# Optimization experiments

Measured on AMD Instinct MI355X. Metric: run time of the kernel, lower is better.

The kernel has to match this reference:

```python
import jax, jax.numpy as jnp
import numpy as np


def setup_inputs() -> dict:
    key = jax.random.key(0)
    B, N, D = 32, 1024, 1024
    x = jax.random.normal(key, (B, N, D), dtype=jnp.float32)
    return {"x": x}


def reference(x) -> jnp.ndarray:
    # query = key = value = x (the module's Linear layers are unused).
    # kl_divs[b,i,j] = KL(softmax(x[b,i]) || softmax(x[b,j])) for i != j, 0 on diag.
    # Since KL(p||p) == 0, the full vectorized KL matrix matches the looped version.
    logp = jax.nn.log_softmax(x, axis=-1)          # [B, N, D]
    p = jnp.exp(logp)                               # softmax(x)
    neg_ent = jnp.sum(p * logp, axis=-1)            # [B, N]  = sum p log p
    cross = jnp.einsum('bid,bjd->bij', p, logp)     # [B, N, N] = sum_d p_i log q_j
    kl = neg_ent[:, :, None] - cross                # [B, N, N]
    attn = jax.nn.softmax(-kl, axis=-1)             # [B, N, N]
    out = jnp.einsum('bij,bjd->bid', attn, x)       # value = x
    return out
```

## Files before the change

kernel.cpp:

```cpp
#include <hip/hip_runtime.h>
#include <hip/hip_bf16.h>
#include <stdint.h>

#define B_ 32
#define N_ 1024
#define D_ 1024

typedef __bf16 bf16x8 __attribute__((ext_vector_type(8)));
typedef float f32x4 __attribute__((ext_vector_type(4)));

static __device__ __forceinline__ unsigned short f2bf(float f) {
    union { float f; unsigned u; } v; v.f = f;
    unsigned r = v.u + 0x7fffu + ((v.u >> 16) & 1u);
    return (unsigned short)(r >> 16);
}

static __device__ __forceinline__ void gld_lds16(const void* g, void* l) {
    __builtin_amdgcn_global_load_lds(
        (const __attribute__((address_space(1))) void*)g,
        (__attribute__((address_space(3))) void*)l, 16, 0, 0);
}

__global__ __launch_bounds__(256) void prep_kernel(const float* __restrict__ x,
        unsigned short* __restrict__ pb, unsigned short* __restrict__ xb,
        float* __restrict__ lse) {
    int row  = blockIdx.x * 4 + (threadIdx.x >> 6);
    int lane = threadIdx.x & 63;
    const float4* xr = (const float4*)(x + (size_t)row * D_);

    float4 v[4];
    #pragma unroll
    for (int q = 0; q < 4; q++) v[q] = xr[lane + 64 * q];

    float m = -1e30f;
    #pragma unroll
    for (int q = 0; q < 4; q++)
        m = fmaxf(m, fmaxf(fmaxf(v[q].x, v[q].y), fmaxf(v[q].z, v[q].w)));
    #pragma unroll
    for (int o = 1; o < 64; o <<= 1) m = fmaxf(m, __shfl_xor(m, o, 64));

    float4 e[4];
    float s = 0.0f;
    #pragma unroll
    for (int q = 0; q < 4; q++) {
        e[q].x = __expf(v[q].x - m); e[q].y = __expf(v[q].y - m);
        e[q].z = __expf(v[q].z - m); e[q].w = __expf(v[q].w - m);
        s += e[q].x + e[q].y + e[q].z + e[q].w;
    }
    #pragma unroll
    for (int o = 1; o < 64; o <<= 1) s += __shfl_xor(s, o, 64);
    float inv = 1.0f / s;

    ushort4* pr = (ushort4*)(pb + (size_t)row * D_);
    ushort4* xw = (ushort4*)(xb + (size_t)row * D_);
    #pragma unroll
    for (int q = 0; q < 4; q++) {
        ushort4 pu, xu;
        pu.x = f2bf(e[q].x * inv); pu.y = f2bf(e[q].y * inv);
        pu.z = f2bf(e[q].z * inv); pu.w = f2bf(e[q].w * inv);
        xu.x = f2bf(v[q].x); xu.y = f2bf(v[q].y);
        xu.z = f2bf(v[q].z); xu.w = f2bf(v[q].w);
        pr[lane + 64 * q] = pu;
        xw[lane + 64 * q] = xu;
    }
    if (lane == 0) lse[row] = m + logf(s);
}

#define SB0() __builtin_amdgcn_sched_barrier(0)

#define STEP(tt, bvC, a0C, bvN, a0N)                                            \
  {                                                                             \
    int brN = (brC == 2) ? 0 : brC + 1;                                         \
    int bw  = (brN == 2) ? 0 : brN + 1;                                         \
    asm volatile("s_waitcnt lgkmcnt(4)" ::: "memory");                          \
    SB0();                                                                      \
    __builtin_amdgcn_s_setprio(1);                                              \
    _Pragma("unroll") for (int i2 = 0; i2 < 4; ++i2)                            \
    _Pragma("unroll") for (int j = 0; j < 4; ++j)                               \
      acc[i2][j] = __builtin_amdgcn_mfma_f32_16x16x32_bf16(a0C[i2], bvC[j],     \
                                                           acc[i2][j], 0, 0, 0);\
    __builtin_amdgcn_s_setprio(0);                                              \
    if ((tt) + 2 < 32) stage(bw, (tt) + 2);                                     \
    asm volatile("s_waitcnt lgkmcnt(0)" ::: "memory");                          \
    if ((tt) < 30)        asm volatile("s_waitcnt vmcnt(4)" ::: "memory");      \
    else if ((tt) == 30)  asm volatile("s_waitcnt vmcnt(0)" ::: "memory");      \
    SB0();                                                                      \
    __builtin_amdgcn_s_barrier();                                               \
    SB0();                                                                      \
    if ((tt) + 1 < 32) {                                                        \
      _Pragma("unroll") for (int j = 0; j < 4; ++j)  bvN[j]  = lB(brN, j);      \
      _Pragma("unroll") for (int i2 = 0; i2 < 4; ++i2) a0N[i2] = lA(brN, 0, i2);\
    }                                                                           \
    SB0();                                                                      \
    __builtin_amdgcn_s_setprio(1);                                              \
    _Pragma("unroll") for (int i2 = 0; i2 < 4; ++i2)                            \
    _Pragma("unroll") for (int j = 0; j < 4; ++j)                               \
      acc[4 + i2][j] = __builtin_amdgcn_mfma_f32_16x16x32_bf16(a1[i2], bvC[j],  \
                                                        acc[4 + i2][j], 0, 0, 0);\
    __builtin_amdgcn_s_setprio(0);                                              \
    if ((tt) + 1 < 32) {                                                        \
      _Pragma("unroll") for (int i2 = 0; i2 < 4; ++i2) a1[i2] = lA(brN, 1, i2); \
    }                                                                           \
    brC = brN;                                                                  \
  }

template<int MODE>
__global__ __launch_bounds__(512, 2) void gemm_bt(const unsigned short* __restrict__ Ag,
        const unsigned short* __restrict__ Bg, void* __restrict__ Cg,
        const float* __restrict__ lse, float* __restrict__ rowsum) {
    const int K = 1024;
    int b = blockIdx.z;
    const unsigned short* A  = Ag + (size_t)b * N_ * K;
    const unsigned short* Bm = Bg + (size_t)b * N_ * K;
    int m0 = blockIdx.y * 256, n0 = blockIdx.x * 256;

    extern __shared__ char lds[];

    int t = threadIdx.x;
    int wave = t >> 6, lane = t & 63;
    int wr = wave >> 2, wc = wave & 3;
    int fm = lane & 15, gf = lane >> 4;

    f32x4 acc[8][4];
    #pragma unroll
    for (int i = 0; i < 8; i++)
        #pragma unroll
        for (int j = 0; j < 4; j++)
            #pragma unroll
            for (int r = 0; r < 4; r++) acc[i][j][r] = 0.0f;

    int rr = t >> 2, s = t & 3;
    int sg = s ^ ((rr >> 1) & 3);
    int rbase = rr + (rr & 64);
    int row0s = rbase;
    int row1s = 64 + rbase;
    const unsigned short* pA0 = A  + (size_t)(m0 + row0s) * K + sg * 8;
    const unsigned short* pA1 = A  + (size_t)(m0 + row1s) * K + sg * 8;
    const unsigned short* pB0 = Bm + (size_t)(n0 + row0s) * K + sg * 8;
    const unsigned short* pB1 = Bm + (size_t)(n0 + row1s) * K + sg * 8;
    int dA0 = row0s * 64 + s * 16;
    int dA1 = row1s * 64 + s * 16;

    auto stage = [&](int bw, int tg) {
        char* ab = lds + bw * 16384;
        char* bb = lds + 49152 + bw * 16384;
        gld_lds16(pA0 + tg * 32, ab + dA0);
        gld_lds16(pA1 + tg * 32, ab + dA1);
        gld_lds16(pB0 + tg * 32, bb + dA0);
        gld_lds16(pB1 + tg * 32, bb + dA1);
    };

    int slot = (gf ^ ((fm >> 1) & 3)) * 16;
    int arow = wr * 128 + fm;
    int brow = wc * 64 + fm;

    auto lA = [&](int br, int q, int i2) {
        return *(const bf16x8*)(lds + br * 16384 + (arow + q * 64 + i2 * 16) * 64 + slot);
    };
    auto lB = [&](int br, int j) {
        return *(const bf16x8*)(lds + 49152 + br * 16384 + (brow + j * 16) * 64 + slot);
    };

    bf16x8 bvA[4], a0A[4], bvB[4], a0B[4], a1[4];

    stage(0, 0);
    stage(1, 1);
    asm volatile("s_waitcnt vmcnt(4)" ::: "memory");
    __builtin_amdgcn_s_barrier();
    SB0();
    #pragma unroll
    for (int j = 0; j < 4; ++j)  bvA[j]  = lB(0, j);
    #pragma unroll
    for (int i2 = 0; i2 < 4; ++i2) a0A[i2] = lA(0, 0, i2);
    SB0();
    #pragma unroll
    for (int i2 = 0; i2 < 4; ++i2) a1[i2] = lA(0, 1, i2);

    int brC = 0;
    for (int tp = 0; tp < 16; ++tp) {
        STEP(2 * tp,     bvA, a0A, bvB, a0B);
        STEP(2 * tp + 1, bvB, a0B, bvA, a0A);
    }

    int cr = (lane >> 4) * 4;
    int cc = lane & 15;

    if (MODE == 0) {
        unsigned short* Co = (unsigned short*)Cg + (size_t)b * (size_t)N_ * N_;
        float lsev[4];
        #pragma unroll
        for (int j = 0; j < 4; j++) lsev[j] = lse[b * N_ + n0 + wc * 64 + j * 16 + cc];
        float rsum[32];
        #pragma unroll
        for (int q = 0; q < 32; q++) rsum[q] = 0.0f;
        #pragma unroll
        for (int i = 0; i < 8; i++) {
            #pragma unroll
            for (int r = 0; r < 4; r++) {
                int row = m0 + wr * 128 + i * 16 + cr + r;
                size_t ro = (size_t)row * N_;
                #pragma unroll
                for (int j = 0; j < 4; j++) {
                    int col = n0 + wc * 64 + j * 16 + cc;
                    float ev = __expf(acc[i][j][r] - lsev[j]);
                    unsigned short eb = f2bf(ev);
                    union { unsigned u; float f; } bk; bk.u = ((unsigned)eb) << 16;
                    Co[ro + col] = eb;
                    rsum[i * 4 + r] += bk.f;
                }
            }
        }
        #pragma unroll
        for (int q = 0; q < 32; q++) {
            float sv = rsum[q];
            sv += __shfl_xor(sv, 1, 64);
            sv += __shfl_xor(sv, 2, 64);
            sv += __shfl_xor(sv, 4, 64);
            sv += __shfl_xor(sv, 8, 64);
            rsum[q] = sv;
        }
        if (cc == 0) {
            #pragma unroll
            for (int q = 0; q < 32; q++) {
                int row = m0 + wr * 128 + (q >> 2) * 16 + cr + (q & 3);
                atomicAdd(&rowsum[b * N_ + row], rsum[q]);
            }
        }
    } else {
        float* Co = (float*)Cg + (size_t)b * (size_t)N_ * N_;
        #pragma unroll
        for (int i = 0; i < 8; i++) {
            #pragma unroll
            for (int r = 0; r < 4; r++) {
                int row = m0 + wr * 128 + i * 16 + cr + r;
                float inv = 1.0f / rowsum[b * N_ + row];
                size_t ro = (size_t)row * N_;
                #pragma unroll
                for (int j = 0; j < 4; j++) {
                    int col = n0 + wc * 64 + j * 16 + cc;
                    Co[ro + col] = acc[i][j][r] * inv;
                }
            }
        }
    }
}

__global__ __launch_bounds__(256) void transpose_kernel(const unsigned short* __restrict__ in,
        unsigned short* __restrict__ out) {
    int b  = blockIdx.z;
    int j0 = blockIdx.y * 64;
    int d0 = blockIdx.x * 64;
    __shared__ unsigned short tile[64][66];
    const unsigned short* ip = in + ((size_t)b * N_ + j0) * D_ + d0;
    int t = threadIdx.x;
    #pragma unroll
    for (int c = t; c < 512; c += 256) {
        int r = c >> 3, col = (c & 7) * 8;
        uint4 val = *(const uint4*)(ip + (size_t)r * D_ + col);
        unsigned int* dst = (unsigned int*)&tile[r][col];
        dst[0] = val.x; dst[1] = val.y; dst[2] = val.z; dst[3] = val.w;
    }
    __syncthreads();
    unsigned short* op = out + ((size_t)b * D_ + d0) * N_ + j0;
    #pragma unroll
    for (int c = t; c < 512; c += 256) {
        int r = c >> 3, col = (c & 7) * 8;
        unsigned short vals[8];
        #pragma unroll
        for (int k = 0; k < 8; k++) vals[k] = tile[col + k][r];
        uint4 o;
        o.x = (unsigned)vals[0] | ((unsigned)vals[1] << 16);
        o.y = (unsigned)vals[2] | ((unsigned)vals[3] << 16);
        o.z = (unsigned)vals[4] | ((unsigned)vals[5] << 16);
        o.w = (unsigned)vals[6] | ((unsigned)vals[7] << 16);
        *(uint4*)(op + (size_t)r * N_ + col) = o;
    }
}

extern "C" void kernel_launch(void* const* d_in, const int* in_sizes, int n_in,
                              void* d_out, int out_size, void* d_ws, size_t ws_size,
                              hipStream_t stream) {
    const float* x = (const float*)d_in[0];
    float* out = (float*)d_out;
    char* ws = (char*)d_ws;

    unsigned short* pb    = (unsigned short*)(ws);
    unsigned short* xb    = (unsigned short*)(ws + 67108864ULL);
    unsigned short* xbT   = (unsigned short*)(ws + 134217728ULL);
    unsigned short* attnE = (unsigned short*)(ws + 201326592ULL);
    float*          lse   = (float*)(ws + 268435456ULL);
    float*          rowsum= (float*)(ws + 268566528ULL);

    hipMemsetAsync(rowsum, 0, B_ * N_ * sizeof(float), stream);
    prep_kernel<<<dim3(B_ * N_ / 4), 256, 0, stream>>>(x, pb, xb, lse);
    transpose_kernel<<<dim3(16, 16, B_), 256, 0, stream>>>(xb, xbT);
    gemm_bt<0><<<dim3(4, 4, B_), 512, 98304, stream>>>(pb, xb, attnE, lse, rowsum);
    gemm_bt<1><<<dim3(4, 4, B_), 512, 98304, stream>>>(attnE, xbT, out, nullptr, rowsum);
}
```

Measured before the change: 420.3 us.

## Restructure GEMM mainloop to 4-stage LDS pipeline with split A/B staging and XCD-aware block remap

The GEMM mainloop moves from a 3-buffer ring with register double-buffering to a 4-buffer LDS ring with three tiles prefetched, and splits each tile's A and B global-to-LDS loads across the two MFMA halves. It adds extra barriers per tile and drops register double buffering, so it relies on deeper prefetch to hide latency. Block indices are also remapped so that blocks sharing a batch land on the same XCD (h&7 interleave), which should improve L2 reuse. LDS usage grows to 128KB per block, which at 2 blocks per CU may limit occupancy.

```diff
diff --git a/kernel.cpp b/kernel.cpp
--- a/kernel.cpp
+++ b/kernel.cpp
@@ -67,41 +67,43 @@
 }
 
 #define SB0() __builtin_amdgcn_sched_barrier(0)
-
-#define STEP(tt, bvC, a0C, bvN, a0N)                                            \
+#define VM8 asm volatile("s_waitcnt vmcnt(8)" ::: "memory")
+#define VM4 asm volatile("s_waitcnt vmcnt(4)" ::: "memory")
+#define VM0 asm volatile("s_waitcnt vmcnt(0)" ::: "memory")
+#define VMN
+
+#define TILE(tt, rB, wB, DOSTAGE, VM)                                           \
   {                                                                             \
-    int brN = (brC == 2) ? 0 : brC + 1;                                         \
-    int bw  = (brN == 2) ? 0 : brN + 1;                                         \
-    asm volatile("s_waitcnt lgkmcnt(4)" ::: "memory");                          \
+    _Pragma("unroll") for (int j = 0; j < 4; ++j)  bv[j] = lB(rB, j);           \
+    _Pragma("unroll") for (int i2 = 0; i2 < 4; ++i2) a0[i2] = lA(rB, 0, i2);    \
+    if (DOSTAGE) stageA(wB, (tt) + 3);                                          \
+    SB0();                                                                      \
+    __builtin_amdgcn_s_barrier();                                               \
+    asm volatile("s_waitcnt lgkmcnt(0)" ::: "memory");                          \
     SB0();                                                                      \
     __builtin_amdgcn_s_setprio(1);                                              \
     _Pragma("unroll") for (int i2 = 0; i2 < 4; ++i2)                            \
-    _Pragma("unroll") for (int j = 0; j < 4; ++j)                               \
-      acc[i2][j] = __builtin_amdgcn_mfma_f32_16x16x32_bf16(a0C[i2], bvC[j],     \
-                                                           acc[i2][j], 0, 0, 0);\
+      _Pragma("unroll") for (int j = 0; j < 4; ++j)                             \
+        acc[i2][j] = __builtin_amdgcn_mfma_f32_16x16x32_bf16(a0[i2], bv[j],     \
+                                                             acc[i2][j], 0, 0, 0); \
     __builtin_amdgcn_s_setprio(0);                                              \
-    if ((tt) + 2 < 32) stage(bw, (tt) + 2);                                     \
+    SB0();                                                                      \
+    __builtin_amdgcn_s_barrier();                                               \
+    _Pragma("unroll") for (int i2 = 0; i2 < 4; ++i2) a1[i2] = lA(rB, 1, i2);    \
+    if (DOSTAGE) stageB(wB, (tt) + 3);                                          \
+    VM;                                                                         \
+    SB0();                                                                      \
+    __builtin_amdgcn_s_barrier();                                               \
     asm volatile("s_waitcnt lgkmcnt(0)" ::: "memory");                          \
-    if ((tt) < 30)        asm volatile("s_waitcnt vmcnt(4)" ::: "memory");      \
-    else if ((tt) == 30)  asm volatile("s_waitcnt vmcnt(0)" ::: "memory");      \
-    SB0();                                                                      \
-    __builtin_amdgcn_s_barrier();                                               \
-    SB0();                                                                      \
-    if ((tt) + 1 < 32) {                                                        \
-      _Pragma("unroll") for (int j = 0; j < 4; ++j)  bvN[j]  = lB(brN, j);      \
-      _Pragma("unroll") for (int i2 = 0; i2 < 4; ++i2) a0N[i2] = lA(brN, 0, i2);\
-    }                                                                           \
     SB0();                                                                      \
     __builtin_amdgcn_s_setprio(1);                                              \
     _Pragma("unroll") for (int i2 = 0; i2 < 4; ++i2)                            \
-    _Pragma("unroll") for (int j = 0; j < 4; ++j)                               \
-      acc[4 + i2][j] = __builtin_amdgcn_mfma_f32_16x16x32_bf16(a1[i2], bvC[j],  \
-                                                        acc[4 + i2][j], 0, 0, 0);\
+      _Pragma("unroll") for (int j = 0; j < 4; ++j)                             \
+        acc[4 + i2][j] = __builtin_amdgcn_mfma_f32_16x16x32_bf16(a1[i2], bv[j], \
+                                                        acc[4 + i2][j], 0, 0, 0); \
     __builtin_amdgcn_s_setprio(0);                                              \
-    if ((tt) + 1 < 32) {                                                        \
-      _Pragma("unroll") for (int i2 = 0; i2 < 4; ++i2) a1[i2] = lA(brN, 1, i2); \
-    }                                                                           \
-    brC = brN;                                                                  \
+    SB0();                                                                      \
+    __builtin_amdgcn_s_barrier();                                               \
   }
 
 template<int MODE>
@@ -109,10 +111,15 @@
         const unsigned short* __restrict__ Bg, void* __restrict__ Cg,
         const float* __restrict__ lse, float* __restrict__ rowsum) {
     const int K = 1024;
-    int b = blockIdx.z;
+
+    int h = blockIdx.x + 4 * blockIdx.y + 16 * blockIdx.z;
+    int l = (h & 7) * 64 + (h >> 3);
+    int b  = l >> 4;
+    int m0 = ((l >> 2) & 3) * 256;
+    int n0 = (l & 3) * 256;
+
     const unsigned short* A  = Ag + (size_t)b * N_ * K;
     const unsigned short* Bm = Bg + (size_t)b * N_ * K;
-    int m0 = blockIdx.y * 256, n0 = blockIdx.x * 256;
 
     extern __shared__ char lds[];
 
@@ -131,56 +138,53 @@
 
     int rr = t >> 2, s = t & 3;
     int sg = s ^ ((rr >> 1) & 3);
-    int rbase = rr + (rr & 64);
-    int row0s = rbase;
-    int row1s = 64 + rbase;
-    const unsigned short* pA0 = A  + (size_t)(m0 + row0s) * K + sg * 8;
-    const unsigned short* pA1 = A  + (size_t)(m0 + row1s) * K + sg * 8;
-    const unsigned short* pB0 = Bm + (size_t)(n0 + row0s) * K + sg * 8;
-    const unsigned short* pB1 = Bm + (size_t)(n0 + row1s) * K + sg * 8;
-    int dA0 = row0s * 64 + s * 16;
-    int dA1 = row1s * 64 + s * 16;
-
-    auto stage = [&](int bw, int tg) {
-        char* ab = lds + bw * 16384;
-        char* bb = lds + 49152 + bw * 16384;
-        gld_lds16(pA0 + tg * 32, ab + dA0);
-        gld_lds16(pA1 + tg * 32, ab + dA1);
-        gld_lds16(pB0 + tg * 32, bb + dA0);
-        gld_lds16(pB1 + tg * 32, bb + dA1);
+    const unsigned short* pA0 = A  + (size_t)(m0 + rr) * K + sg * 8;
+    const unsigned short* pA1 = A  + (size_t)(m0 + 128 + rr) * K + sg * 8;
+    const unsigned short* pB0 = Bm + (size_t)(n0 + rr) * K + sg * 8;
+    const unsigned short* pB1 = Bm + (size_t)(n0 + 128 + rr) * K + sg * 8;
+    int d0 = rr * 64 + s * 16;
+    int d1 = (128 + rr) * 64 + s * 16;
+
+    auto stageA = [&](int w, int tg) {
+        char* ab = lds + w * 32768;
+        gld_lds16(pA0 + tg * 32, ab + d0);
+        gld_lds16(pA1 + tg * 32, ab + d1);
     };
+    auto stageB = [&](int w, int tg) {
+        char* bb = lds + w * 32768 + 16384;
+        gld_lds16(pB0 + tg * 32, bb + d0);
+        gld_lds16(pB1 + tg * 32, bb + d1);
+    };
 
     int slot = (gf ^ ((fm >> 1) & 3)) * 16;
-    int arow = wr * 128 + fm;
-    int brow = wc * 64 + fm;
-
     auto lA = [&](int br, int q, int i2) {
-        return *(const bf16x8*)(lds + br * 16384 + (arow + q * 64 + i2 * 16) * 64 + slot);
+        return *(const bf16x8*)(lds + br * 32768 +
+                 (wr * 128 + (q * 4 + i2) * 16 + fm) * 64 + slot);
     };
     auto lB = [&](int br, int j) {
-        return *(const bf16x8*)(lds + 49152 + br * 16384 + (brow + j * 16) * 64 + slot);
+        return *(const bf16x8*)(lds + br * 32768 + 16384 +
+                 (wc * 64 + j * 16 + fm) * 64 + slot);
     };
 
-    bf16x8 bvA[4], a0A[4], bvB[4], a0B[4], a1[4];
-
-    stage(0, 0);
-    stage(1, 1);
-    asm volatile("s_waitcnt vmcnt(4)" ::: "memory");
+    bf16x8 bv[4], a0[4], a1[4];
+
+    stageA(0, 0); stageB(0, 0);
+    stageA(1, 1); stageB(1, 1);
+    stageA(2, 2); stageB(2, 2);
+    VM8;
     __builtin_amdgcn_s_barrier();
-    SB0();
-    #pragma unroll
-    for (int j = 0; j < 4; ++j)  bvA[j]  = lB(0, j);
-    #pragma unroll
-    for (int i2 = 0; i2 < 4; ++i2) a0A[i2] = lA(0, 0, i2);
-    SB0();
-    #pragma unroll
-    for (int i2 = 0; i2 < 4; ++i2) a1[i2] = lA(0, 1, i2);
-
-    int brC = 0;
-    for (int tp = 0; tp < 16; ++tp) {
-        STEP(2 * tp,     bvA, a0A, bvB, a0B);
-        STEP(2 * tp + 1, bvB, a0B, bvA, a0A);
-    }
+
+    for (int tp = 0; tp < 7; ++tp) {
+        int t0 = tp * 4;
+        TILE(t0 + 0, 0, 3, 1, VM8);
+        TILE(t0 + 1, 1, 0, 1, VM8);
+        TILE(t0 + 2, 2, 1, 1, VM8);
+        TILE(t0 + 3, 3, 2, 1, VM8);
+    }
+    TILE(28, 0, 3, 1, VM8);
+    TILE(29, 1, 0, 0, VM4);
+    TILE(30, 2, 1, 0, VM0);
+    TILE(31, 3, 2, 0, VMN);
 
     int cr = (lane >> 4) * 4;
     int cc = lane & 15;
@@ -294,6 +298,6 @@
     hipMemsetAsync(rowsum, 0, B_ * N_ * sizeof(float), stream);
     prep_kernel<<<dim3(B_ * N_ / 4), 256, 0, stream>>>(x, pb, xb, lse);
     transpose_kernel<<<dim3(16, 16, B_), 256, 0, stream>>>(xb, xbT);
-    gemm_bt<0><<<dim3(4, 4, B_), 512, 98304, stream>>>(pb, xb, attnE, lse, rowsum);
-    gemm_bt<1><<<dim3(4, 4, B_), 512, 98304, stream>>>(attnE, xbT, out, nullptr, rowsum);
-}
+    gemm_bt<0><<<dim3(4, 4, B_), 512, 131072, stream>>>(pb, xb, attnE, lse, rowsum);
+    gemm_bt<1><<<dim3(4, 4, B_), 512, 131072, stream>>>(attnE, xbT, out, nullptr, rowsum);
+}
```

Result: no change. 419.9 us (-0.1%).
